# Kernel optimization log

Hardware: AMD Instinct MI355X
Metric: run time of the kernel (lower is better)

Reference implementation:

```python
import jax, jax.numpy as jnp
import numpy as np
import math

B, S, D, H = 4, 2048, 1024, 16
HD = D // H
EPS = 1e-10


def setup_inputs() -> dict:
    key = jax.random.key(0)
    kx, kq, kk, kv, ko = jax.random.split(key, 5)
    x = jax.random.normal(kx, (B, S, D), dtype=jnp.float32)
    # causal additive mask: 0 on/below diagonal, -1e9 above
    mask = jnp.where(jnp.triu(jnp.ones((S, S), dtype=bool), k=1), -1e9, 0.0).astype(jnp.float32)
    scale = 1.0 / math.sqrt(D)
    Wq = jax.random.normal(kq, (D, D), dtype=jnp.float32) * scale
    Wk = jax.random.normal(kk, (D, D), dtype=jnp.float32) * scale
    Wv = jax.random.normal(kv, (D, D), dtype=jnp.float32) * scale
    Wo = jax.random.normal(ko, (D, D), dtype=jnp.float32) * scale
    return {"x": x, "mask": mask, "Wq": Wq, "Wk": Wk, "Wv": Wv, "Wo": Wo}


def _nirmalya_softmax(t):
    # faithful to original: plain exp (no max-subtraction), eps in denominator
    p1 = jnp.exp(t)
    return p1 / (jnp.sum(p1, axis=-1, keepdims=True) + EPS)


def reference(x, mask, Wq, Wk, Wv, Wo):
    b, s, d = x.shape
    # torch Linear (bias=False): y = x @ W.T
    def proj(W):
        y = jnp.einsum('bsd,ed->bse', x, W)
        return y.reshape(b, s, H, HD).transpose(0, 2, 1, 3)  # [b,h,s,hd]
    q, k, v = proj(Wq), proj(Wk), proj(Wv)
    scores = jnp.einsum('bhqd,bhkd->bhqk', q, k) / math.sqrt(HD)
    scores = scores + mask  # broadcast over batch/heads
    attn = _nirmalya_softmax(scores)
    out = jnp.einsum('bhqk,bhkd->bhqd', attn, v)
    out = out.transpose(0, 2, 1, 3).reshape(b, s, d)
    return jnp.einsum('bsd,ed->bse', out, Wo)
```

## Files before the change

kernel.cpp:

```cpp
#include <hip/hip_runtime.h>
#include <hip/hip_bf16.h>

typedef __bf16 bf16;
typedef __attribute__((ext_vector_type(8))) __bf16 bf16x8;
typedef __attribute__((ext_vector_type(4))) float f32x4;
typedef __attribute__((ext_vector_type(16))) float f32x16;
typedef __attribute__((ext_vector_type(2))) unsigned int u32x2;
typedef __attribute__((ext_vector_type(4))) unsigned int u32x4;

#define MFMA16(a, b, c) __builtin_amdgcn_mfma_f32_16x16x32_bf16((a), (b), (c), 0, 0, 0)
#define MFMA32(a, b, c) __builtin_amdgcn_mfma_f32_32x32x16_bf16((a), (b), (c), 0, 0, 0)

#define GLOAD_LDS16(gp, lp)                                                              \
  __builtin_amdgcn_global_load_lds(                                                      \
      (const __attribute__((address_space(1))) unsigned int*)(gp),                       \
      (__attribute__((address_space(3))) unsigned int*)(lp), 16, 0, 0)

#define BAR()   __builtin_amdgcn_s_barrier()
#define LGKM0() asm volatile("s_waitcnt lgkmcnt(0)" ::: "memory")
#define VMC(n)  asm volatile("s_waitcnt vmcnt(" #n ")" ::: "memory")
#define PRIO1() __builtin_amdgcn_s_setprio(1)
#define PRIO0() __builtin_amdgcn_s_setprio(0)

__global__ __launch_bounds__(256) void cvt_all(const float* __restrict__ x,
                                               const float* __restrict__ wq,
                                               const float* __restrict__ wk,
                                               const float* __restrict__ wv,
                                               const float* __restrict__ wo,
                                               bf16* __restrict__ xb,
                                               bf16* __restrict__ wqkv,
                                               bf16* __restrict__ wob) {
  constexpr int NXC = 8388608 / 8;
  constexpr int NWC = 1048576 / 8;
  constexpr int TOT = NXC + 4 * NWC;
  for (int c = blockIdx.x * 256 + threadIdx.x; c < TOT; c += gridDim.x * 256) {
    const float* src; bf16* dst; int idx;
    if (c < NXC) { src = x; dst = xb; idx = c; }
    else {
      int c2 = c - NXC; int wsel = c2 >> 17; idx = c2 & (NWC - 1);
      src = wsel == 0 ? wq : wsel == 1 ? wk : wsel == 2 ? wv : wo;
      dst = wsel < 3 ? wqkv + (size_t)wsel * 1048576 : wob;
    }
    float4 v0 = reinterpret_cast<const float4*>(src)[idx * 2];
    float4 v1 = reinterpret_cast<const float4*>(src)[idx * 2 + 1];
    bf16x8 o;
    o[0] = (bf16)v0.x; o[1] = (bf16)v0.y; o[2] = (bf16)v0.z; o[3] = (bf16)v0.w;
    o[4] = (bf16)v1.x; o[5] = (bf16)v1.y; o[6] = (bf16)v1.z; o[7] = (bf16)v1.w;
    reinterpret_cast<bf16x8*>(dst)[idx] = o;
  }
}

#define MMA8(BF, MH, NH)                                                                 \
  _Pragma("unroll") for (int mi = 0; mi < 2; ++mi)                                       \
  _Pragma("unroll") for (int ni = 0; ni < 2; ++ni)                                       \
  _Pragma("unroll") for (int ks = 0; ks < 2; ++ks)                                       \
      acc[(MH) * 2 + mi][(NH) * 2 + ni] =                                                \
          MFMA16(af[mi][ks], (BF)[ni][ks], acc[(MH) * 2 + mi][(NH) * 2 + ni]);

template <int MODE, int NT>
__global__ __launch_bounds__(512, 1) void gemm8(const bf16* __restrict__ A,
                                                const bf16* __restrict__ B,
                                                void* __restrict__ Cv,
                                                bf16* __restrict__ VT) {
  constexpr int K = 1024;
  __shared__ bf16 smem[49152];
  const int tid = threadIdx.x, lane = tid & 63, w = tid >> 6;
  const int l15 = lane & 15, l16 = lane >> 4;
  const int wr = w >> 2, wc = w & 3;
  const int lin = blockIdx.x;
  const int idx = lin >> 3;
  const int mt = (lin & 7) * 8 + idx / NT;
  const int nt = idx % NT;
  const int bm0 = mt * 128, bn0 = nt * 256;

  auto stA = [&](int buf, int t, int j) {
    const int r = j * 64 + (tid >> 3);
    const int g = (tid & 7) ^ (r & 7);
    GLOAD_LDS16(&A[(size_t)(bm0 + r) * K + t * 64 + g * 8],
                &smem[buf * 8192 + j * 4096 + tid * 8]);
  };
  auto stB = [&](int buf, int t, int j) {
    const int r = j * 64 + (tid >> 3);
    const int g = (tid & 7) ^ (r & 7);
    GLOAD_LDS16(&B[(size_t)(bn0 + r) * K + t * 64 + g * 8],
                &smem[16384 + buf * 16384 + j * 4096 + tid * 8]);
  };
  bf16x8 af[2][2], b0[2][2], b1[2][2];
  auto ldA = [&](int buf, int mh, bf16x8 (&dst)[2][2]) {
#pragma unroll
    for (int mi = 0; mi < 2; ++mi)
#pragma unroll
      for (int ks = 0; ks < 2; ++ks)
        dst[mi][ks] = *reinterpret_cast<const bf16x8*>(
            &smem[buf * 8192 + (wr * 64 + mh * 32 + mi * 16 + l15) * 64 +
                  (((ks * 4 + l16) ^ (l15 & 7)) * 8)]);
  };
  auto ldB = [&](int buf, int nh, bf16x8 (&dst)[2][2]) {
#pragma unroll
    for (int ni = 0; ni < 2; ++ni)
#pragma unroll
      for (int ks = 0; ks < 2; ++ks)
        dst[ni][ks] = *reinterpret_cast<const bf16x8*>(
            &smem[16384 + buf * 16384 + (wc * 64 + nh * 32 + ni * 16 + l15) * 64 +
                  (((ks * 4 + l16) ^ (l15 & 7)) * 8)]);
  };

  f32x4 acc[4][4] = {};

  stA(0, 0, 0); stA(0, 0, 1);
  stB(0, 0, 0); stB(0, 0, 1); stB(0, 0, 2); stB(0, 0, 3);
  stA(1, 1, 0); stA(1, 1, 1);
  stB(1, 1, 0); stB(1, 1, 1); stB(1, 1, 2); stB(1, 1, 3);
  VMC(6); BAR();

#pragma unroll 1
  for (int it = 0; it < K / 128; ++it) {
    const int t0 = 2 * it;
    const bool last = (it == K / 128 - 1);
    ldA(0, 0, af); ldB(0, 0, b0);
    BAR(); LGKM0();
    PRIO1(); MMA8(b0, 0, 0); PRIO0();
    BAR();
    ldB(0, 1, b1);
    BAR(); LGKM0();
    PRIO1(); MMA8(b1, 0, 1); PRIO0();
    BAR();
    ldA(0, 1, af);
    BAR(); LGKM0();
    PRIO1(); MMA8(b1, 1, 1); PRIO0();
    BAR();
    if (!last) {
      stA(0, t0 + 2, 0); stA(0, t0 + 2, 1);
      stB(0, t0 + 2, 0); stB(0, t0 + 2, 1); stB(0, t0 + 2, 2); stB(0, t0 + 2, 3);
    }
    PRIO1(); MMA8(b0, 1, 0); PRIO0();
    if (last) { VMC(0); } else { VMC(6); }
    BAR();
    ldA(1, 0, af); ldB(1, 0, b0);
    BAR(); LGKM0();
    PRIO1(); MMA8(b0, 0, 0); PRIO0();
    BAR();
    ldB(1, 1, b1);
    BAR(); LGKM0();
    PRIO1(); MMA8(b1, 0, 1); PRIO0();
    BAR();
    ldA(1, 1, af);
    BAR(); LGKM0();
    PRIO1(); MMA8(b1, 1, 1); PRIO0();
    BAR();
    if (!last) {
      stA(1, t0 + 3, 0); stA(1, t0 + 3, 1);
      stB(1, t0 + 3, 0); stB(1, t0 + 3, 1); stB(1, t0 + 3, 2); stB(1, t0 + 3, 3);
    }
    PRIO1(); MMA8(b0, 1, 0); PRIO0();
    if (!last) VMC(6);
    BAR();
  }

  if constexpr (MODE == 0) {
#pragma unroll
    for (int i = 0; i < 4; ++i)
#pragma unroll
      for (int j = 0; j < 4; ++j)
#pragma unroll
        for (int r = 0; r < 4; ++r) {
          const size_t row = bm0 + wr * 64 + (i >> 1) * 32 + (i & 1) * 16 + l16 * 4 + r;
          const size_t col = bn0 + wc * 64 + (j >> 1) * 32 + (j & 1) * 16 + l15;
          reinterpret_cast<float*>(Cv)[row * (NT * 256) + col] = acc[i][j][r];
        }
  } else {
    if (bn0 < 2048) {
#pragma unroll
      for (int i = 0; i < 4; ++i)
#pragma unroll
        for (int j = 0; j < 4; ++j)
#pragma unroll
          for (int r = 0; r < 4; ++r) {
            const size_t row = bm0 + wr * 64 + (i >> 1) * 32 + (i & 1) * 16 + l16 * 4 + r;
            const size_t col = bn0 + wc * 64 + (j >> 1) * 32 + (j & 1) * 16 + l15;
            float v = acc[i][j][r];
            if (col < 1024) v *= 0.18033688011112042f;
            reinterpret_cast<bf16*>(Cv)[row * 2048 + col] = (bf16)v;
          }
    } else {
#pragma unroll
      for (int i = 0; i < 4; ++i)
#pragma unroll
        for (int j = 0; j < 4; ++j)
#pragma unroll
          for (int r = 0; r < 4; ++r) {
            const int m = wr * 64 + (i >> 1) * 32 + (i & 1) * 16 + l16 * 4 + r;
            const int n = wc * 64 + (j >> 1) * 32 + (j & 1) * 16 + l15;
            smem[n * 136 + m] = (bf16)acc[i][j][r];
          }
      BAR();
      const int n = tid >> 1, half = tid & 1;
      const size_t vbase = ((size_t)(bm0 >> 11) * 1024 + (bn0 - 2048 + n)) * 2048 +
                           (bm0 & 2047) + half * 64;
#pragma unroll
      for (int k = 0; k < 8; ++k) {
        bf16x8 v = *reinterpret_cast<const bf16x8*>(&smem[n * 136 + half * 64 + k * 8]);
        *reinterpret_cast<bf16x8*>(&VT[vbase + k * 8]) = v;
      }
    }
  }
}

constexpr int S_ = 2048, H_ = 16, LDQK = 2048;

__global__ __launch_bounds__(128, 2) void attn_kernel(const bf16* __restrict__ QK,
                                                      const bf16* __restrict__ VT,
                                                      bf16* __restrict__ AO) {
  __shared__ bf16 Ks[2][64 * 64];
  __shared__ bf16 Vs[2][64 * 64];
  const int tid = threadIdx.x, lane = tid & 63, w = tid >> 6;
  const int l31 = lane & 31, hi = lane >> 5;
  const int x7 = l31 & 7;
  const int bh = blockIdx.x, b = bh >> 4, h = bh & (H_ - 1);
  const int pairid = blockIdx.y;
  const size_t qoff = (size_t)b * S_ * LDQK + h * 64;
  const size_t koff = qoff + 1024;
  const size_t voff = (size_t)bh * 64 * LDQK;
  const size_t aoff = (size_t)b * S_ * 1024 + h * 64;

  auto stage = [&](int t) {
    const int kv0 = t * 64, bs = t & 1;
#pragma unroll
    for (int i = 0; i < 4; ++i) {
      const int c = tid + 128 * i;
      const int row = c >> 3, gs = (c & 7) ^ (row & 7);
      GLOAD_LDS16(&QK[koff + (size_t)(kv0 + row) * LDQK + gs * 8], &Ks[bs][c * 8]);
      GLOAD_LDS16(&VT[voff + (size_t)row * LDQK + kv0 + gs * 8], &Vs[bs][c * 8]);
    }
  };

#pragma unroll 1
  for (int half = 0; half < 2; ++half) {
    const int j = half ? (31 - pairid) : pairid;
    const int qbase = j * 64 + w * 32;
    const int ntiles = j + 1;
    const int qg = qbase + l31;

    bf16x8 qf[4];
#pragma unroll
    for (int ks = 0; ks < 4; ++ks)
      qf[ks] = *reinterpret_cast<const bf16x8*>(
          &QK[qoff + (size_t)qg * LDQK + ks * 16 + hi * 8]);

    f32x16 oT[2] = {};
    float rs = 0.0f;

    stage(0);
    VMC(0); BAR();

#pragma unroll 1
    for (int t = 0; t < ntiles; ++t) {
      if (t + 1 < ntiles) stage(t + 1);
      const int bs = t & 1;
      const int kv0 = t * 64;

      f32x16 sc[2] = {};
      PRIO1();
#pragma unroll
      for (int ks = 0; ks < 4; ++ks) {
        bf16x8 kf0 = *reinterpret_cast<bf16x8*>(
            &Ks[bs][l31 * 64 + (((ks * 2 + hi) ^ x7) * 8)]);
        bf16x8 kf1 = *reinterpret_cast<bf16x8*>(
            &Ks[bs][(32 + l31) * 64 + (((ks * 2 + hi) ^ x7) * 8)]);
        sc[0] = MFMA32(kf0, qf[ks], sc[0]);
        sc[1] = MFMA32(kf1, qf[ks], sc[1]);
      }
      PRIO0();

      const bool diag = (t == j);
      const int hi4 = hi * 4;
#pragma unroll
      for (int hh = 0; hh < 2; ++hh)
#pragma unroll
        for (int r = 0; r < 16; ++r) {
          float e = exp2f(sc[hh][r]);
          if (diag) {
            const int kvg = kv0 + hh * 32 + (r & 3) + 8 * (r >> 2) + hi4;
            e = (kvg <= qg) ? e : 0.0f;
          }
          rs += e;
          sc[hh][r] = e;
        }

      u32x4 pf[4];
#pragma unroll
      for (int hh = 0; hh < 2; ++hh)
#pragma unroll
        for (int q4 = 0; q4 < 2; ++q4) {
          unsigned x0, x1, y0, y1;
          asm("v_cvt_pk_bf16_f32 %0, %1, %2" : "=v"(x0)
              : "v"(sc[hh][q4 * 8 + 0]), "v"(sc[hh][q4 * 8 + 1]));
          asm("v_cvt_pk_bf16_f32 %0, %1, %2" : "=v"(x1)
              : "v"(sc[hh][q4 * 8 + 2]), "v"(sc[hh][q4 * 8 + 3]));
          asm("v_cvt_pk_bf16_f32 %0, %1, %2" : "=v"(y0)
              : "v"(sc[hh][q4 * 8 + 4]), "v"(sc[hh][q4 * 8 + 5]));
          asm("v_cvt_pk_bf16_f32 %0, %1, %2" : "=v"(y1)
              : "v"(sc[hh][q4 * 8 + 6]), "v"(sc[hh][q4 * 8 + 7]));
          asm("v_permlane32_swap_b32 %0, %1" : "+v"(x0), "+v"(y0));
          asm("v_permlane32_swap_b32 %0, %1" : "+v"(x1), "+v"(y1));
          pf[hh * 2 + q4][0] = x0; pf[hh * 2 + q4][1] = x1;
          pf[hh * 2 + q4][2] = y0; pf[hh * 2 + q4][3] = y1;
        }

      PRIO1();
#pragma unroll
      for (int ks = 0; ks < 4; ++ks) {
        bf16x8 vt0 = *reinterpret_cast<bf16x8*>(
            &Vs[bs][l31 * 64 + (((ks * 2 + hi) ^ x7) * 8)]);
        bf16x8 vt1 = *reinterpret_cast<bf16x8*>(
            &Vs[bs][(32 + l31) * 64 + (((ks * 2 + hi) ^ x7) * 8)]);
        oT[0] = MFMA32(vt0, *reinterpret_cast<bf16x8*>(&pf[ks]), oT[0]);
        oT[1] = MFMA32(vt1, *reinterpret_cast<bf16x8*>(&pf[ks]), oT[1]);
      }
      PRIO0();

      VMC(0); BAR();
    }

    const float rst = rs + __shfl_xor(rs, 32);
    const float inv = 1.0f / (rst + 1e-10f);

    bf16* lo = &Ks[0][0] + w * 2048;
#pragma unroll
    for (int dh = 0; dh < 2; ++dh)
#pragma unroll
      for (int rq = 0; rq < 4; ++rq) {
        const float v0 = oT[dh][rq * 4 + 0] * inv, v1 = oT[dh][rq * 4 + 1] * inv;
        const float v2 = oT[dh][rq * 4 + 2] * inv, v3 = oT[dh][rq * 4 + 3] * inv;
        unsigned d0, d1;
        asm("v_cvt_pk_bf16_f32 %0, %1, %2" : "=v"(d0) : "v"(v0), "v"(v1));
        asm("v_cvt_pk_bf16_f32 %0, %1, %2" : "=v"(d1) : "v"(v2), "v"(v3));
        u32x2 dd; dd[0] = d0; dd[1] = d1;
        *reinterpret_cast<u32x2*>(
            &lo[l31 * 64 + (((dh * 4 + rq) ^ x7) * 8) + hi * 4]) = dd;
      }
#pragma unroll
    for (int jj = 0; jj < 4; ++jj) {
      const int gran = lane + 64 * jj;
      const int qr = gran >> 3, g = gran & 7;
      bf16x8 vv = *reinterpret_cast<bf16x8*>(&lo[qr * 64 + ((g ^ (qr & 7)) * 8)]);
      *reinterpret_cast<bf16x8*>(
          &AO[aoff + (size_t)(j * 64 + w * 32 + qr) * 1024 + g * 8]) = vv;
    }
    LGKM0(); BAR();
  }
}

extern "C" void kernel_launch(void* const* d_in, const int* in_sizes, int n_in,
                              void* d_out, int out_size, void* d_ws, size_t ws_size,
                              hipStream_t stream) {
  const float* x  = (const float*)d_in[0];
  const float* Wq = (const float*)d_in[2];
  const float* Wk = (const float*)d_in[3];
  const float* Wv = (const float*)d_in[4];
  const float* Wo = (const float*)d_in[5];

  constexpr int B = 4, S = 2048, D = 1024;
  constexpr size_t nx = (size_t)B * S * D;
  constexpr size_t nw = (size_t)D * D;

  char* ws = (char*)d_ws;
  bf16* xb    = (bf16*)ws;
  bf16* Wqkvb = xb + nx;
  bf16* Wob   = Wqkvb + 3 * nw;
  bf16* QKb   = Wob + nw;
  bf16* VTb   = QKb + (size_t)B * S * 2048;
  bf16* AOb   = VTb + nx;

  cvt_all<<<2048, 256, 0, stream>>>(x, Wq, Wk, Wv, Wo, xb, Wqkvb, Wob);

  gemm8<2, 12><<<768, 512, 0, stream>>>(xb, Wqkvb, QKb, VTb);

  attn_kernel<<<dim3(B * H_, 16), 128, 0, stream>>>(QKb, VTb, AOb);

  gemm8<0, 4><<<256, 512, 0, stream>>>(AOb, Wob, d_out, nullptr);
}
```

Baseline: 174.6 us.

## Software-pipeline attention loop: overlap next tile's QK^T with current softmax/PV

Restructures the KV loop so the QK^T MFMAs for tile t+1 are issued before the exp/convert/PV work for tile t. K tiles are prefetched two tiles ahead and V tiles one ahead, with separate staging lambdas. Two ping-ponged score register sets let matrix and vector work interleave, and the loop is manually unrolled by two. It also replaces exp2f with a raw v_exp_f32. The cost is more live registers for the second score buffer and a more complex staging order.

New measurement: 159.8 us. 8.5% less time.

```diff
diff --git a/kernel.cpp b/kernel.cpp
--- a/kernel.cpp
+++ b/kernel.cpp
@@ -223,13 +223,21 @@
   const size_t voff = (size_t)bh * 64 * LDQK;
   const size_t aoff = (size_t)b * S_ * 1024 + h * 64;
 
-  auto stage = [&](int t) {
+  auto stK = [&](int t) {
     const int kv0 = t * 64, bs = t & 1;
 #pragma unroll
     for (int i = 0; i < 4; ++i) {
       const int c = tid + 128 * i;
       const int row = c >> 3, gs = (c & 7) ^ (row & 7);
       GLOAD_LDS16(&QK[koff + (size_t)(kv0 + row) * LDQK + gs * 8], &Ks[bs][c * 8]);
+    }
+  };
+  auto stV = [&](int t) {
+    const int kv0 = t * 64, bs = t & 1;
+#pragma unroll
+    for (int i = 0; i < 4; ++i) {
+      const int c = tid + 128 * i;
+      const int row = c >> 3, gs = (c & 7) ^ (row & 7);
       GLOAD_LDS16(&VT[voff + (size_t)row * LDQK + kv0 + gs * 8], &Vs[bs][c * 8]);
     }
   };
@@ -249,17 +257,12 @@
 
     f32x16 oT[2] = {};
     float rs = 0.0f;
-
-    stage(0);
-    VMC(0); BAR();
-
-#pragma unroll 1
-    for (int t = 0; t < ntiles; ++t) {
-      if (t + 1 < ntiles) stage(t + 1);
+    f32x16 scA[2], scB[2];
+
+    auto qkt = [&](int t, f32x16 (&sc)[2]) {
       const int bs = t & 1;
-      const int kv0 = t * 64;
-
-      f32x16 sc[2] = {};
+      f32x16 zz = {};
+      sc[0] = zz; sc[1] = zz;
       PRIO1();
 #pragma unroll
       for (int ks = 0; ks < 4; ++ks) {
@@ -271,14 +274,18 @@
         sc[1] = MFMA32(kf1, qf[ks], sc[1]);
       }
       PRIO0();
-
+    };
+
+    auto softpv = [&](int t, f32x16 (&sc)[2]) {
       const bool diag = (t == j);
+      const int kv0 = t * 64;
       const int hi4 = hi * 4;
 #pragma unroll
       for (int hh = 0; hh < 2; ++hh)
 #pragma unroll
         for (int r = 0; r < 16; ++r) {
-          float e = exp2f(sc[hh][r]);
+          float e;
+          asm("v_exp_f32 %0, %1" : "=v"(e) : "v"(sc[hh][r]));
           if (diag) {
             const int kvg = kv0 + hh * 32 + (r & 3) + 8 * (r >> 2) + hi4;
             e = (kvg <= qg) ? e : 0.0f;
@@ -286,7 +293,6 @@
           rs += e;
           sc[hh][r] = e;
         }
-
       u32x4 pf[4];
 #pragma unroll
       for (int hh = 0; hh < 2; ++hh)
@@ -306,7 +312,7 @@
           pf[hh * 2 + q4][0] = x0; pf[hh * 2 + q4][1] = x1;
           pf[hh * 2 + q4][2] = y0; pf[hh * 2 + q4][3] = y1;
         }
-
+      const int bs = t & 1;
       PRIO1();
 #pragma unroll
       for (int ks = 0; ks < 4; ++ks) {
@@ -318,8 +324,25 @@
         oT[1] = MFMA32(vt1, *reinterpret_cast<bf16x8*>(&pf[ks]), oT[1]);
       }
       PRIO0();
-
+    };
+
+    auto step = [&](int t, f32x16 (&cur)[2], f32x16 (&nxt)[2]) {
+      if (t + 2 < ntiles) stK(t + 2);
+      if (t + 1 < ntiles) { stV(t + 1); qkt(t + 1, nxt); }
+      softpv(t, cur);
       VMC(0); BAR();
+    };
+
+    stK(0); stV(0);
+    if (ntiles > 1) stK(1);
+    VMC(0); BAR();
+    qkt(0, scA);
+    BAR();
+
+#pragma unroll 1
+    for (int t = 0; t < ntiles; t += 2) {
+      step(t, scA, scB);
+      if (t + 1 < ntiles) step(t + 1, scB, scA);
     }
 
     const float rst = rs + __shfl_xor(rs, 32);
```
